# Kernel optimization log

Measured on AMD Instinct MI355X. Metric: run time of the kernel, lower is better.

## Reference

```python
import jax, jax.numpy as jnp
import numpy as np

NUM_HEADS = 16
EPS = 1e-6  # torch LayerNorm default is 1e-5; module uses nn.LayerNorm default
LN_EPS = 1e-5


def layer_norm(x, w, b, eps=LN_EPS):
    # normalize over last dim (head_dim), matching infer_layer_norm
    mu = jnp.mean(x, axis=-1, keepdims=True)
    xc = x - mu
    var = jnp.mean(xc * xc, axis=-1, keepdims=True)
    return xc / jnp.sqrt(var + eps) * w + b


def setup_inputs() -> dict:
    key = jax.random.key(0)
    ks = jax.random.split(key, 4)
    B, N, C = 2, 4096, 1024
    H = NUM_HEADS
    D = C // H
    x = jax.random.normal(ks[0], (B, N, C), dtype=jnp.float32)
    qkv_w = jax.random.normal(ks[1], (3 * C, C), dtype=jnp.float32) * (C ** -0.5)
    qkv_b = jax.random.normal(ks[2], (3 * C,), dtype=jnp.float32) * 0.02
    q_norm_w = jnp.ones((D,), dtype=jnp.float32)
    q_norm_b = jnp.zeros((D,), dtype=jnp.float32)
    k_norm_w = jnp.ones((D,), dtype=jnp.float32)
    k_norm_b = jnp.zeros((D,), dtype=jnp.float32)
    proj_w = jax.random.normal(ks[3], (C, C), dtype=jnp.float32) * (C ** -0.5)
    proj_b = jnp.zeros((C,), dtype=jnp.float32)
    return {"x": x, "qkv_w": qkv_w, "qkv_b": qkv_b,
            "q_norm_w": q_norm_w, "q_norm_b": q_norm_b,
            "k_norm_w": k_norm_w, "k_norm_b": k_norm_b,
            "proj_w": proj_w, "proj_b": proj_b}


def reference(x, qkv_w, qkv_b, q_norm_w, q_norm_b, k_norm_w, k_norm_b, proj_w, proj_b):
    B, N, C = x.shape
    H = NUM_HEADS
    D = C // H
    scale = D ** -0.5
    # QKV projection: torch Linear uses y = x @ W^T + b
    qkv = x @ qkv_w.T + qkv_b                      # [B,N,3C]
    qkv = qkv.reshape(B, N, 3, H, D).transpose(2, 0, 3, 1, 4)  # [3,B,H,N,D]
    q, k, v = qkv[0], qkv[1], qkv[2]
    # per-head qk layernorm
    q = layer_norm(q, q_norm_w, q_norm_b)
    k = layer_norm(k, k_norm_w, k_norm_b)
    # scaled dot product attention
    attn = jnp.einsum('bhqd,bhkd->bhqk', q * scale, k)
    attn = jax.nn.softmax(attn, axis=-1)
    out = jnp.einsum('bhqk,bhkd->bhqd', attn, v)   # [B,H,N,D]
    out = out.transpose(0, 2, 1, 3).reshape(B, N, C)
    return out @ proj_w.T + proj_b
```

## Files before the change

### kernel.cpp

```cpp
#include <hip/hip_runtime.h>
#include <hip/hip_bf16.h>

#define NB 2
#define NN 4096
#define NC 1024
#define NH 16
#define ND 64
#define NM (NB*NN)
#define NK 1024
#define J_QKV 3072
#define QSCALE 0.18033688011112042f

typedef unsigned short u16;
typedef unsigned int   u32;
typedef __attribute__((ext_vector_type(8)))  __bf16 bf16x8;
typedef __attribute__((ext_vector_type(4)))  float  f32x4;
typedef __attribute__((ext_vector_type(16))) float  f32x16;

__device__ __forceinline__ u16 f2bf(float f) {
    unsigned int i = __builtin_bit_cast(unsigned int, f);
    unsigned int lsb = (i >> 16) & 1u;
    i += 0x7fffu + lsb;
    return (u16)(i >> 16);
}
__device__ __forceinline__ float fast_exp2(float x) {
#if __has_builtin(__builtin_amdgcn_exp2f)
    return __builtin_amdgcn_exp2f(x);
#else
    return exp2f(x);
#endif
}
__device__ __forceinline__ u32 pkbf(float a, float b) {
    u32 r;
    asm("v_cvt_pk_bf16_f32 %0, %1, %2" : "=v"(r) : "v"(a), "v"(b));
    return r;
}
typedef struct { u32 x, y; } u32pair;
__device__ __forceinline__ u32pair swap32(u32 a, u32 b) {
#if __has_builtin(__builtin_amdgcn_permlane32_swap)
    auto r = __builtin_amdgcn_permlane32_swap((int)a, (int)b, false, false);
    u32pair o; o.x = (u32)r[0]; o.y = (u32)r[1]; return o;
#else
    const bool hi = (threadIdx.x & 32) != 0;
    u32 as = (u32)__shfl_xor((int)a, 32);
    u32 bs = (u32)__shfl_xor((int)b, 32);
    u32pair o; o.x = hi ? bs : a; o.y = hi ? b : as; return o;
#endif
}

__device__ __forceinline__ void glds16(const u16* g, u16* l) {
    __builtin_amdgcn_global_load_lds(
        (const __attribute__((address_space(1))) u32*)g,
        (__attribute__((address_space(3))) u32*)l, 16, 0, 0);
}

__global__ __launch_bounds__(256) void cvt_bf16(
    const float* __restrict__ in, u16* __restrict__ out)
{
    const size_t i = ((size_t)blockIdx.x * 256 + threadIdx.x) * 8;
    const float4 a = *(const float4*)(in + i);
    const float4 b = *(const float4*)(in + i + 4);
    union { u16 h[8]; uint4 v; } u;
    u.h[0] = f2bf(a.x); u.h[1] = f2bf(a.y); u.h[2] = f2bf(a.z); u.h[3] = f2bf(a.w);
    u.h[4] = f2bf(b.x); u.h[5] = f2bf(b.y); u.h[6] = f2bf(b.z); u.h[7] = f2bf(b.w);
    *(uint4*)(out + i) = u.v;
}

template<int MODE>
__global__ __launch_bounds__(256) void gemm_nt(
    const u16* __restrict__ A, const u16* __restrict__ W,
    const float* __restrict__ bias,
    const float* __restrict__ qw, const float* __restrict__ qb,
    const float* __restrict__ kw, const float* __restrict__ kb,
    void* __restrict__ outv)
{
    __shared__ __align__(16) u16 As[128][32];
    __shared__ __align__(16) u16 Bs[128][32];
    const int t = threadIdx.x;
    const int w = t >> 6, lane = t & 63;
    const int jb = blockIdx.x * 128;
    const int m0 = blockIdx.y * 128;
    const int wr = (w >> 1) * 64, wc = (w & 1) * 64;
    const int srow = t >> 2, skc = (t & 3) * 8;
    const u16* ap0 = A + (size_t)(m0 + srow) * NK + skc;
    const u16* ap1 = ap0 + (size_t)64 * NK;
    const u16* wp0 = W + (size_t)(jb + srow) * NK + skc;
    const u16* wp1 = wp0 + (size_t)64 * NK;
    u16* as0 = &As[srow][skc];      u16* as1 = &As[srow + 64][skc];
    u16* bs0 = &Bs[srow][skc];      u16* bs1 = &Bs[srow + 64][skc];
    const int fm = lane & 15, fk = 8 * (lane >> 4);
    f32x4 acc[4][4];
    #pragma unroll
    for (int i = 0; i < 4; ++i)
        #pragma unroll
        for (int j = 0; j < 4; ++j) acc[i][j] = (f32x4){0.f, 0.f, 0.f, 0.f};

    for (int kt = 0; kt < NK / 32; ++kt) {
        const int ko = kt * 32;
        glds16(ap0 + ko, as0);
        glds16(ap1 + ko, as1);
        glds16(wp0 + ko, bs0);
        glds16(wp1 + ko, bs1);
        __syncthreads();
        bf16x8 af[4], bfr[4];
        #pragma unroll
        for (int i = 0; i < 4; ++i) af[i]  = *(const bf16x8*)&As[wr + 16 * i + fm][fk];
        #pragma unroll
        for (int j = 0; j < 4; ++j) bfr[j] = *(const bf16x8*)&Bs[wc + 16 * j + fm][fk];
        #pragma unroll
        for (int i = 0; i < 4; ++i)
            #pragma unroll
            for (int j = 0; j < 4; ++j)
                acc[i][j] = __builtin_amdgcn_mfma_f32_16x16x32_bf16(af[i], bfr[j], acc[i][j], 0, 0, 0);
        __syncthreads();
    }
    const int c16 = lane & 15;
    float bv[4];
    #pragma unroll
    for (int j = 0; j < 4; ++j) bv[j] = bias[jb + wc + 16 * j + c16];
    #pragma unroll
    for (int i = 0; i < 4; ++i)
        #pragma unroll
        for (int j = 0; j < 4; ++j)
            #pragma unroll
            for (int r = 0; r < 4; ++r) acc[i][j][r] += bv[j];
    if (MODE == 0) {
        const int s = jb >> 10;
        if (s < 2) {
            const float* lw = s ? kw : qw;
            const float* lb = s ? kb : qb;
            float lwv[4], lbv[4];
            #pragma unroll
            for (int j = 0; j < 4; ++j) {
                lwv[j] = lw[16 * j + c16]; lbv[j] = lb[16 * j + c16];
            }
            #pragma unroll
            for (int i = 0; i < 4; ++i)
                #pragma unroll
                for (int r = 0; r < 4; ++r) {
                    float sum = acc[i][0][r] + acc[i][1][r] + acc[i][2][r] + acc[i][3][r];
                    #pragma unroll
                    for (int off = 1; off < 16; off <<= 1) sum += __shfl_xor(sum, off);
                    const float mu = sum * (1.0f / 64.0f);
                    float v2 = 0.f;
                    #pragma unroll
                    for (int j = 0; j < 4; ++j) { const float dd = acc[i][j][r] - mu; v2 += dd * dd; }
                    #pragma unroll
                    for (int off = 1; off < 16; off <<= 1) v2 += __shfl_xor(v2, off);
                    const float rstd = rsqrtf(v2 * (1.0f / 64.0f) + 1e-5f);
                    #pragma unroll
                    for (int j = 0; j < 4; ++j) {
                        float y = (acc[i][j][r] - mu) * rstd * lwv[j] + lbv[j];
                        if (s == 0) y *= QSCALE;
                        acc[i][j][r] = y;
                    }
                }
        }
        u16* out = (u16*)outv;
        const int r0 = 4 * (lane >> 4);
        #pragma unroll
        for (int j = 0; j < 4; ++j) {
            const int col = jb + wc + 16 * j + c16;
            const int ss = col >> 10, hh = (col >> 6) & 15, d = col & 63;
            #pragma unroll
            for (int i = 0; i < 4; ++i)
                #pragma unroll
                for (int r = 0; r < 4; ++r) {
                    const int row = m0 + wr + 16 * i + r0 + r;
                    const int b = row >> 12, n = row & 4095;
                    out[((((size_t)ss * NB + b) * NH + hh) * NN + n) * ND + d] = f2bf(acc[i][j][r]);
                }
        }
    } else {
        float* out = (float*)outv;
        const int r0 = 4 * (lane >> 4);
        #pragma unroll
        for (int i = 0; i < 4; ++i)
            #pragma unroll
            for (int r = 0; r < 4; ++r) {
                const int row = m0 + wr + 16 * i + r0 + r;
                #pragma unroll
                for (int j = 0; j < 4; ++j)
                    out[(size_t)row * NC + jb + wc + 16 * j + c16] = acc[i][j][r];
            }
    }
}

__global__ __launch_bounds__(256, 2) void attn_mfma(
    const u16* __restrict__ qkv, u16* __restrict__ aout)
{
    __shared__ __align__(16) u16 Ks[2][64][72];
    __shared__ __align__(16) u16 Vt[2][64][72];
    const int bid  = blockIdx.x;
    const int qblk = bid & 15;
    const int bh   = bid >> 4;
    const int b = bh >> 4, hh = bh & 15;
    const size_t plane = (size_t)NB * NH * NN * ND;
    const size_t base  = ((size_t)(b * NH + hh)) * NN * ND;
    const u16* qp = qkv + base;
    const u16* kp = qkv + plane + base;
    const u16* vp = qkv + 2 * plane + base;
    const int t = threadIdx.x, w = t >> 6, lane = t & 63;
    const int half = lane >> 5, m32 = lane & 31;
    const int q0 = qblk * 256 + 64 * w;

    bf16x8 qf[2][4];
    #pragma unroll
    for (int s = 0; s < 2; ++s) {
        const u16* qrow = qp + (size_t)(q0 + 32 * s + m32) * ND + 8 * half;
        #pragma unroll
        for (int kt = 0; kt < 4; ++kt) qf[s][kt] = *(const bf16x8*)(qrow + 16 * kt);
    }
    f32x16 O[2][2], z;
    #pragma unroll
    for (int r = 0; r < 16; ++r) { O[0][0][r] = 0.f; O[0][1][r] = 0.f;
                                   O[1][0][r] = 0.f; O[1][1][r] = 0.f; z[r] = 0.f; }
    float lpart[2] = {0.f, 0.f};

    const int dgK = 16 * w;
    const int kp2 = t & 31, dgV = (t >> 5) * 8;
    const u16* ksrc = kp + (size_t)lane * ND + dgK;
    const u16* vsrc = vp + (size_t)(2 * kp2) * ND + dgV;

    uint4 kr0, kr1, vre, vro;
    kr0 = *(const uint4*)(ksrc);
    kr1 = *(const uint4*)(ksrc + 8);
    vre = *(const uint4*)(vsrc);
    vro = *(const uint4*)(vsrc + ND);
    {
        *(uint4*)&Ks[0][lane][dgK]     = kr0;
        *(uint4*)&Ks[0][lane][dgK + 8] = kr1;
        const u32* ew = (const u32*)&vre;
        const u32* ow = (const u32*)&vro;
        #pragma unroll
        for (int d = 0; d < 4; ++d) {
            u32 lo = __builtin_amdgcn_perm(ow[d], ew[d], 0x05040100u);
            u32 hi = __builtin_amdgcn_perm(ow[d], ew[d], 0x07060302u);
            *(u32*)&Vt[0][dgV + 2 * d][2 * kp2]     = lo;
            *(u32*)&Vt[0][dgV + 2 * d + 1][2 * kp2] = hi;
        }
    }
    __syncthreads();

    union W8 { u32 wd[4]; bf16x8 f; };

    for (int kb = 0; kb < NN / 64; ++kb) {
        const int cur = kb & 1, nxt = cur ^ 1;
        const bool more = (kb + 1) < (NN / 64);
        if (more) {
            const u16* ks2 = ksrc + (size_t)(kb + 1) * 64 * ND;
            kr0 = *(const uint4*)ks2;
            kr1 = *(const uint4*)(ks2 + 8);
            const u16* vs2 = vsrc + (size_t)(kb + 1) * 64 * ND;
            vre = *(const uint4*)vs2;
            vro = *(const uint4*)(vs2 + ND);
        }
        f32x16 sT0[2], sT1[2];
        __builtin_amdgcn_s_setprio(1);
        {
            bf16x8 k0 = *(const bf16x8*)&Ks[cur][m32][8 * half];
            bf16x8 k1 = *(const bf16x8*)&Ks[cur][32 + m32][8 * half];
            sT0[0] = __builtin_amdgcn_mfma_f32_32x32x16_bf16(k0, qf[0][0], z, 0, 0, 0);
            sT0[1] = __builtin_amdgcn_mfma_f32_32x32x16_bf16(k1, qf[0][0], z, 0, 0, 0);
        }
        #pragma unroll
        for (int kt = 1; kt < 4; ++kt) {
            bf16x8 k0 = *(const bf16x8*)&Ks[cur][m32][16 * kt + 8 * half];
            bf16x8 k1 = *(const bf16x8*)&Ks[cur][32 + m32][16 * kt + 8 * half];
            sT0[0] = __builtin_amdgcn_mfma_f32_32x32x16_bf16(k0, qf[0][kt], sT0[0], 0, 0, 0);
            sT0[1] = __builtin_amdgcn_mfma_f32_32x32x16_bf16(k1, qf[0][kt], sT0[1], 0, 0, 0);
        }
        {
            bf16x8 k0 = *(const bf16x8*)&Ks[cur][m32][8 * half];
            bf16x8 k1 = *(const bf16x8*)&Ks[cur][32 + m32][8 * half];
            sT1[0] = __builtin_amdgcn_mfma_f32_32x32x16_bf16(k0, qf[1][0], z, 0, 0, 0);
            sT1[1] = __builtin_amdgcn_mfma_f32_32x32x16_bf16(k1, qf[1][0], z, 0, 0, 0);
        }
        #pragma unroll
        for (int kt = 1; kt < 4; ++kt) {
            bf16x8 k0 = *(const bf16x8*)&Ks[cur][m32][16 * kt + 8 * half];
            bf16x8 k1 = *(const bf16x8*)&Ks[cur][32 + m32][16 * kt + 8 * half];
            sT1[0] = __builtin_amdgcn_mfma_f32_32x32x16_bf16(k0, qf[1][kt], sT1[0], 0, 0, 0);
            sT1[1] = __builtin_amdgcn_mfma_f32_32x32x16_bf16(k1, qf[1][kt], sT1[1], 0, 0, 0);
        }
        __builtin_amdgcn_s_setprio(0);
        W8 pa0[4], pa1[4];
        {
            float ss0 = 0.f, ss1 = 0.f;
            #pragma unroll
            for (int kh = 0; kh < 2; ++kh) {
                float p[16];
                #pragma unroll
                for (int r = 0; r < 16; ++r) p[r] = fast_exp2(sT0[kh][r]);
                #pragma unroll
                for (int r = 0; r < 8; ++r) { ss0 += p[r]; ss1 += p[8 + r]; }
                u32 c[4][2];
                #pragma unroll
                for (int g = 0; g < 4; ++g) {
                    c[g][0] = pkbf(p[4 * g + 0], p[4 * g + 1]);
                    c[g][1] = pkbf(p[4 * g + 2], p[4 * g + 3]);
                }
                #pragma unroll
                for (int par = 0; par < 2; ++par) {
                    u32pair wA = swap32(c[2 * par][0], c[2 * par + 1][0]);
                    u32pair wB = swap32(c[2 * par][1], c[2 * par + 1][1]);
                    const int kt = 2 * kh + par;
                    pa0[kt].wd[0] = wA.x;
                    pa0[kt].wd[1] = wB.x;
                    pa0[kt].wd[2] = wA.y;
                    pa0[kt].wd[3] = wB.y;
                }
            }
            lpart[0] += ss0 + ss1;
        }
        __builtin_amdgcn_s_setprio(1);
        #pragma unroll
        for (int kt = 0; kt < 4; ++kt) {
            bf16x8 v0 = *(const bf16x8*)&Vt[cur][m32][16 * kt + 8 * half];
            bf16x8 v1 = *(const bf16x8*)&Vt[cur][32 + m32][16 * kt + 8 * half];
            O[0][0] = __builtin_amdgcn_mfma_f32_32x32x16_bf16(pa0[kt].f, v0, O[0][0], 0, 0, 0);
            O[0][1] = __builtin_amdgcn_mfma_f32_32x32x16_bf16(pa0[kt].f, v1, O[0][1], 0, 0, 0);
        }
        __builtin_amdgcn_s_setprio(0);
        {
            float ss0 = 0.f, ss1 = 0.f;
            #pragma unroll
            for (int kh = 0; kh < 2; ++kh) {
                float p[16];
                #pragma unroll
                for (int r = 0; r < 16; ++r) p[r] = fast_exp2(sT1[kh][r]);
                #pragma unroll
                for (int r = 0; r < 8; ++r) { ss0 += p[r]; ss1 += p[8 + r]; }
                u32 c[4][2];
                #pragma unroll
                for (int g = 0; g < 4; ++g) {
                    c[g][0] = pkbf(p[4 * g + 0], p[4 * g + 1]);
                    c[g][1] = pkbf(p[4 * g + 2], p[4 * g + 3]);
                }
                #pragma unroll
                for (int par = 0; par < 2; ++par) {
                    u32pair wA = swap32(c[2 * par][0], c[2 * par + 1][0]);
                    u32pair wB = swap32(c[2 * par][1], c[2 * par + 1][1]);
                    const int kt = 2 * kh + par;
                    pa1[kt].wd[0] = wA.x;
                    pa1[kt].wd[1] = wB.x;
                    pa1[kt].wd[2] = wA.y;
                    pa1[kt].wd[3] = wB.y;
                }
            }
            lpart[1] += ss0 + ss1;
        }
        __builtin_amdgcn_s_setprio(1);
        #pragma unroll
        for (int kt = 0; kt < 4; ++kt) {
            bf16x8 v0 = *(const bf16x8*)&Vt[cur][m32][16 * kt + 8 * half];
            bf16x8 v1 = *(const bf16x8*)&Vt[cur][32 + m32][16 * kt + 8 * half];
            O[1][0] = __builtin_amdgcn_mfma_f32_32x32x16_bf16(pa1[kt].f, v0, O[1][0], 0, 0, 0);
            O[1][1] = __builtin_amdgcn_mfma_f32_32x32x16_bf16(pa1[kt].f, v1, O[1][1], 0, 0, 0);
        }
        __builtin_amdgcn_s_setprio(0);
        if (more) {
            *(uint4*)&Ks[nxt][lane][dgK]     = kr0;
            *(uint4*)&Ks[nxt][lane][dgK + 8] = kr1;
            const u32* ew = (const u32*)&vre;
            const u32* ow = (const u32*)&vro;
            #pragma unroll
            for (int d = 0; d < 4; ++d) {
                u32 lo = __builtin_amdgcn_perm(ow[d], ew[d], 0x05040100u);
                u32 hi = __builtin_amdgcn_perm(ow[d], ew[d], 0x07060302u);
                *(u32*)&Vt[nxt][dgV + 2 * d][2 * kp2]     = lo;
                *(u32*)&Vt[nxt][dgV + 2 * d + 1][2 * kp2] = hi;
            }
            __syncthreads();
        }
    }
    #pragma unroll
    for (int s = 0; s < 2; ++s) {
        const float tot = lpart[s] + __shfl_xor(lpart[s], 32);
        #pragma unroll
        for (int r = 0; r < 16; ++r) {
            const int qq = (r & 3) + 8 * (r >> 2) + 4 * half;
            const float inv = 1.0f / __shfl(tot, qq);
            const int row = q0 + 32 * s + qq;
            u16* dst = aout + ((size_t)(b * NN + row)) * NC + hh * 64;
            dst[m32]      = f2bf(O[s][0][r] * inv);
            dst[32 + m32] = f2bf(O[s][1][r] * inv);
        }
    }
}

extern "C" void kernel_launch(void* const* d_in, const int* in_sizes, int n_in,
                              void* d_out, int out_size, void* d_ws, size_t ws_size,
                              hipStream_t stream) {
    const float* x     = (const float*)d_in[0];
    const float* qkv_w = (const float*)d_in[1];
    const float* qkv_b = (const float*)d_in[2];
    const float* q_nw  = (const float*)d_in[3];
    const float* q_nb  = (const float*)d_in[4];
    const float* k_nw  = (const float*)d_in[5];
    const float* k_nb  = (const float*)d_in[6];
    const float* p_w   = (const float*)d_in[7];
    const float* p_b   = (const float*)d_in[8];
    float* out = (float*)d_out;
    u16* qkv    = (u16*)d_ws;
    u16* x_bf   = qkv + (size_t)3 * NB * NH * NN * ND;
    u16* attn_o = x_bf;
    u16* w_bf   = x_bf + (size_t)NM * NC;
    u16* pw_bf  = w_bf + (size_t)J_QKV * NK;

    cvt_bf16<<<(NM * NC) / 2048, 256, 0, stream>>>(x, x_bf);
    cvt_bf16<<<(J_QKV * NK) / 2048, 256, 0, stream>>>(qkv_w, w_bf);
    cvt_bf16<<<(NC * NK) / 2048, 256, 0, stream>>>(p_w, pw_bf);

    gemm_nt<0><<<dim3(J_QKV / 128, NM / 128), 256, 0, stream>>>(
        x_bf, w_bf, qkv_b, q_nw, q_nb, k_nw, k_nb, qkv);
    attn_mfma<<<NB * NH * (NN / 256), 256, 0, stream>>>(qkv, attn_o);
    gemm_nt<1><<<dim3(NC / 128, NM / 128), 256, 0, stream>>>(
        attn_o, pw_bf, p_b, q_nw, q_nb, k_nw, k_nb, out);
}
```

Measured before the change: 363.9 us.

## Deepen GEMM K-step to 64 and remap blocks across XCDs

Each main-loop iteration of the GEMM now loads a 64-wide K slice into two LDS halves, so it does half as many barrier pairs per tile. The launch grid is flattened to 1D, and block indices are permuted so that consecutive tiles land on the same XCD, which should improve L2 reuse of the A and W rows. A launch_bounds occupancy hint of 3 blocks is also added. LDS per block doubles to 32KB, which may limit occupancy.

```diff
diff --git a/kernel.cpp b/kernel.cpp
--- a/kernel.cpp
+++ b/kernel.cpp
@@ -66,28 +66,35 @@
     *(uint4*)(out + i) = u.v;
 }
 
-template<int MODE>
-__global__ __launch_bounds__(256) void gemm_nt(
+template<int MODE, int NJB>
+__global__ __launch_bounds__(256, 3) void gemm_nt(
     const u16* __restrict__ A, const u16* __restrict__ W,
     const float* __restrict__ bias,
     const float* __restrict__ qw, const float* __restrict__ qb,
     const float* __restrict__ kw, const float* __restrict__ kb,
     void* __restrict__ outv)
 {
-    __shared__ __align__(16) u16 As[128][32];
-    __shared__ __align__(16) u16 Bs[128][32];
+    __shared__ __align__(16) u16 AsL[128][32];
+    __shared__ __align__(16) u16 AsH[128][32];
+    __shared__ __align__(16) u16 BsL[128][32];
+    __shared__ __align__(16) u16 BsH[128][32];
     const int t = threadIdx.x;
     const int w = t >> 6, lane = t & 63;
-    const int jb = blockIdx.x * 128;
-    const int m0 = blockIdx.y * 128;
+    const int nb  = blockIdx.x;
+    const int cpx = gridDim.x >> 3;
+    const int nb2 = (nb & 7) * cpx + (nb >> 3);
+    const int jb  = (nb2 % NJB) * 128;
+    const int m0  = (nb2 / NJB) * 128;
     const int wr = (w >> 1) * 64, wc = (w & 1) * 64;
     const int srow = t >> 2, skc = (t & 3) * 8;
     const u16* ap0 = A + (size_t)(m0 + srow) * NK + skc;
     const u16* ap1 = ap0 + (size_t)64 * NK;
     const u16* wp0 = W + (size_t)(jb + srow) * NK + skc;
     const u16* wp1 = wp0 + (size_t)64 * NK;
-    u16* as0 = &As[srow][skc];      u16* as1 = &As[srow + 64][skc];
-    u16* bs0 = &Bs[srow][skc];      u16* bs1 = &Bs[srow + 64][skc];
+    u16* asl0 = &AsL[srow][skc];    u16* asl1 = &AsL[srow + 64][skc];
+    u16* ash0 = &AsH[srow][skc];    u16* ash1 = &AsH[srow + 64][skc];
+    u16* bsl0 = &BsL[srow][skc];    u16* bsl1 = &BsL[srow + 64][skc];
+    u16* bsh0 = &BsH[srow][skc];    u16* bsh1 = &BsH[srow + 64][skc];
     const int fm = lane & 15, fk = 8 * (lane >> 4);
     f32x4 acc[4][4];
     #pragma unroll
@@ -95,23 +102,41 @@
         #pragma unroll
         for (int j = 0; j < 4; ++j) acc[i][j] = (f32x4){0.f, 0.f, 0.f, 0.f};
 
-    for (int kt = 0; kt < NK / 32; ++kt) {
-        const int ko = kt * 32;
-        glds16(ap0 + ko, as0);
-        glds16(ap1 + ko, as1);
-        glds16(wp0 + ko, bs0);
-        glds16(wp1 + ko, bs1);
+    for (int kt = 0; kt < NK / 64; ++kt) {
+        const int ko = kt * 64;
+        glds16(ap0 + ko, asl0);
+        glds16(ap1 + ko, asl1);
+        glds16(ap0 + ko + 32, ash0);
+        glds16(ap1 + ko + 32, ash1);
+        glds16(wp0 + ko, bsl0);
+        glds16(wp1 + ko, bsl1);
+        glds16(wp0 + ko + 32, bsh0);
+        glds16(wp1 + ko + 32, bsh1);
         __syncthreads();
-        bf16x8 af[4], bfr[4];
-        #pragma unroll
-        for (int i = 0; i < 4; ++i) af[i]  = *(const bf16x8*)&As[wr + 16 * i + fm][fk];
-        #pragma unroll
-        for (int j = 0; j < 4; ++j) bfr[j] = *(const bf16x8*)&Bs[wc + 16 * j + fm][fk];
-        #pragma unroll
-        for (int i = 0; i < 4; ++i)
-            #pragma unroll
-            for (int j = 0; j < 4; ++j)
-                acc[i][j] = __builtin_amdgcn_mfma_f32_16x16x32_bf16(af[i], bfr[j], acc[i][j], 0, 0, 0);
+        {
+            bf16x8 af[4], bfr[4];
+            #pragma unroll
+            for (int i = 0; i < 4; ++i) af[i]  = *(const bf16x8*)&AsL[wr + 16 * i + fm][fk];
+            #pragma unroll
+            for (int j = 0; j < 4; ++j) bfr[j] = *(const bf16x8*)&BsL[wc + 16 * j + fm][fk];
+            #pragma unroll
+            for (int i = 0; i < 4; ++i)
+                #pragma unroll
+                for (int j = 0; j < 4; ++j)
+                    acc[i][j] = __builtin_amdgcn_mfma_f32_16x16x32_bf16(af[i], bfr[j], acc[i][j], 0, 0, 0);
+        }
+        {
+            bf16x8 af[4], bfr[4];
+            #pragma unroll
+            for (int i = 0; i < 4; ++i) af[i]  = *(const bf16x8*)&AsH[wr + 16 * i + fm][fk];
+            #pragma unroll
+            for (int j = 0; j < 4; ++j) bfr[j] = *(const bf16x8*)&BsH[wc + 16 * j + fm][fk];
+            #pragma unroll
+            for (int i = 0; i < 4; ++i)
+                #pragma unroll
+                for (int j = 0; j < 4; ++j)
+                    acc[i][j] = __builtin_amdgcn_mfma_f32_16x16x32_bf16(af[i], bfr[j], acc[i][j], 0, 0, 0);
+        }
         __syncthreads();
     }
     const int c16 = lane & 15;
@@ -412,9 +437,9 @@
     cvt_bf16<<<(J_QKV * NK) / 2048, 256, 0, stream>>>(qkv_w, w_bf);
     cvt_bf16<<<(NC * NK) / 2048, 256, 0, stream>>>(p_w, pw_bf);
 
-    gemm_nt<0><<<dim3(J_QKV / 128, NM / 128), 256, 0, stream>>>(
+    gemm_nt<0, J_QKV / 128><<<(J_QKV / 128) * (NM / 128), 256, 0, stream>>>(
         x_bf, w_bf, qkv_b, q_nw, q_nb, k_nw, k_nb, qkv);
     attn_mfma<<<NB * NH * (NN / 256), 256, 0, stream>>>(qkv, attn_o);
-    gemm_nt<1><<<dim3(NC / 128, NM / 128), 256, 0, stream>>>(
+    gemm_nt<1, NC / 128><<<(NC / 128) * (NM / 128), 256, 0, stream>>>(
         attn_o, pw_bf, p_b, q_nw, q_nb, k_nw, k_nb, out);
 }
```

Result: faster. 331.8 us (-8.8%).
